# Optimization experiments

Measured on AMD Instinct MI355X. Metric: run time of the kernel, lower is better.

## Reference

```python
import jax, jax.numpy as jnp
import numpy as np

I, H = 256, 512  # input_sz, hidden_sz
MU_MIN, MU_MAX, STD_MIN = 1e-6, 1e6, 1e-6


def _xavier(key, shape):
    fan_in, fan_out = shape[1], shape[0]
    a = jnp.sqrt(6.0 / (fan_in + fan_out)).astype(jnp.float32)
    return jax.random.uniform(key, shape, jnp.float32, -a, a)


def setup_inputs() -> dict:
    key = jax.random.key(0)
    ks = jax.random.split(key, 6)
    B, S = 64, 512
    x = jax.random.normal(ks[0], (B, S, I), jnp.float32)
    eps = jax.random.normal(ks[1], (S + 1, B, H), jnp.float32)
    W_ih = _xavier(ks[2], (4 * H, I))   # torch LSTM weight_ih_l0, gate order i,f,g,o
    W_hh = _xavier(ks[3], (4 * H, H))
    b_ih = jnp.zeros((4 * H,), jnp.float32)
    b_hh = jnp.zeros((4 * H,), jnp.float32)
    G = _xavier(ks[4], (H, 2 * H))      # Gaussian_Sampler gauss_parameter_generator
    return {"x": x, "eps": eps, "W_ih": W_ih, "W_hh": W_hh, "b_ih": b_ih, "b_hh": b_hh, "G": G}


def _sample(c, G, eps_t):
    # c: [B,H]; stats = c @ G -> [B,2H]
    stats = c @ G
    mu = jnp.clip(stats[:, :H], MU_MIN, MU_MAX)
    std = jnp.clip(jax.nn.softplus(stats[:, H:]), STD_MIN)
    return mu + eps_t * std, mu, std


def reference(x, eps, W_ih, W_hh, b_ih, b_hh, G):
    B, S, _ = x.shape
    h0 = jnp.zeros((B, H), x.dtype)
    c0 = jnp.zeros((B, H), x.dtype)
    # initial sampling of cell state (uses eps[0])
    c0_s, mu0, std0 = _sample(c0, G, eps[0])

    def step(carry, inp):
        h, c = carry
        x_t, eps_t = inp  # [B,I], [B,H]
        gates = x_t @ W_ih.T + b_ih + h @ W_hh.T + b_hh  # [B,4H]
        i_g = jax.nn.sigmoid(gates[:, 0 * H:1 * H])
        f_g = jax.nn.sigmoid(gates[:, 1 * H:2 * H])
        g_g = jnp.tanh(gates[:, 2 * H:3 * H])
        o_g = jax.nn.sigmoid(gates[:, 3 * H:4 * H])
        c_new = f_g * c + i_g * g_g
        h_new = o_g * jnp.tanh(c_new)
        c_s, mu, std = _sample(c_new, G, eps_t)
        return (h_new, c_s), (h_new, mu, std)

    xs = (jnp.swapaxes(x, 0, 1), eps[1:])  # [S,B,I], [S,B,H]
    (h_f, c_f), (hs, mus, stds) = jax.lax.scan(step, (h0, c0_s), xs)
    hidden_seq = jnp.swapaxes(hs, 0, 1)  # [B,S,H]
    c_mus = jnp.swapaxes(jnp.concatenate([mu0[None], mus], 0), 0, 1)    # [B,S+1,H]
    c_stds = jnp.swapaxes(jnp.concatenate([std0[None], stds], 0), 0, 1)  # [B,S+1,H]
    return hidden_seq, c_mus, c_stds, h_f, c_f
```

## Files before the change

### kernel.cpp

```cpp
#include <hip/hip_runtime.h>
#include <hip/hip_bf16.h>
#include <math.h>

#define I_DIM 256
#define H_DIM 512
#define B_DIM 64
#define S_DIM 512
#define SH    (S_DIM * H_DIM)
#define S1H   ((S_DIM + 1) * H_DIM)
#define BH    (B_DIM * H_DIM)
#define NGRP  4
#define GWG   64
#define NWG_TOT (NGRP * GWG)

typedef __bf16 bf16_t;
typedef bf16_t bf16x8 __attribute__((ext_vector_type(8)));
typedef float  f32x4  __attribute__((ext_vector_type(4)));
typedef float  f32x2  __attribute__((ext_vector_type(2)));

__device__ __forceinline__ float sigm_(float x) { return 1.0f / (1.0f + __expf(-x)); }
__device__ __forceinline__ float tanh_(float x) {
    x = fminf(fmaxf(x, -15.f), 15.f);
    float e = __expf(-2.f * x);
    return (1.f - e) / (1.f + e);
}
__device__ __forceinline__ float softplus_(float x) {
    return (x > 20.0f) ? x : log1pf(__expf(x));
}
__device__ __forceinline__ unsigned short bfbits_(float f) {
    return __builtin_bit_cast(unsigned short, (bf16_t)f);
}

__device__ __forceinline__ bf16x8 ld_frag(const bf16_t* base, int elem_idx) {
    return *reinterpret_cast<const bf16x8*>(base + elem_idx);
}

__global__ void k_init(bf16_t* __restrict__ hbuf0, unsigned int* __restrict__ bar,
                       float* __restrict__ out_cmu, float* __restrict__ out_cstd) {
    const int i = blockIdx.x * 256 + threadIdx.x;
    hbuf0[i] = (bf16_t)0.0f;
    const int b = i >> 9, j = i & 511;
    out_cmu [b * S1H + j] = 1e-6f;
    out_cstd[b * S1H + j] = 0.69314718055994531f;
    if (i < NWG_TOT) bar[i] = 0u;
}

__global__ __launch_bounds__(64, 1) void k_persist(
    const float* __restrict__ x, const float* __restrict__ eps,
    const float* __restrict__ W_ih, const float* __restrict__ W_hh,
    const float* __restrict__ b_ih, const float* __restrict__ b_hh,
    const float* __restrict__ Gm,
    bf16_t* __restrict__ hb0, bf16_t* __restrict__ hb1,
    bf16_t* __restrict__ cn0, bf16_t* __restrict__ cn1,
    unsigned int* __restrict__ bar,
    float* __restrict__ out_hidden, float* __restrict__ out_cmu,
    float* __restrict__ out_cstd, float* __restrict__ out_hf,
    float* __restrict__ out_cf)
{
    __shared__ __align__(16) unsigned short s_wih[8][2][64][8];
    __shared__ __align__(16) unsigned short s_gfr[16][64][8];
    __shared__ char s_pad[64 * 1024];
    if (x == nullptr) ((volatile char*)s_pad)[threadIdx.x] = 1;

    const int wc = blockIdx.x & 63;
    const int g  = blockIdx.x >> 6;
    const int l  = threadIdx.x;
    const int lr = l & 15;
    const int kq = l >> 4;
    const int nsub   = lr & 7;
    const int ghalf  = lr >> 3;
    const int mycell = wc * 8 + nsub;
    const int col0 = ghalf * H_DIM + mycell;
    const int col1 = 1024 + col0;
    const int gcol = ghalf * H_DIM + mycell;
    const int row0 = g * 16 + kq * 4;
    const int arow = g * 16 + lr;
    unsigned int* barg = bar + g * GWG;

    bf16x8 whh0[16], whh1[16];
    #pragma unroll
    for (int kt = 0; kt < 16; ++kt) {
        const float* p0 = W_hh + (size_t)col0 * H_DIM + kt * 32 + kq * 8;
        const float* p1 = W_hh + (size_t)col1 * H_DIM + kt * 32 + kq * 8;
        bf16x8 f0, f1;
        #pragma unroll
        for (int j = 0; j < 8; ++j) { f0[j] = (bf16_t)p0[j]; f1[j] = (bf16_t)p1[j]; }
        whh0[kt] = f0; whh1[kt] = f1;
    }
    #pragma unroll
    for (int kt = 0; kt < 8; ++kt) {
        const float* p0 = W_ih + (size_t)col0 * I_DIM + kt * 32 + kq * 8;
        const float* p1 = W_ih + (size_t)col1 * I_DIM + kt * 32 + kq * 8;
        bf16x8 f0, f1;
        #pragma unroll
        for (int j = 0; j < 8; ++j) { f0[j] = (bf16_t)p0[j]; f1[j] = (bf16_t)p1[j]; }
        *reinterpret_cast<bf16x8*>(&s_wih[kt][0][l][0]) = f0;
        *reinterpret_cast<bf16x8*>(&s_wih[kt][1][l][0]) = f1;
    }
    #pragma unroll
    for (int kt = 0; kt < 16; ++kt) {
        bf16x8 f;
        #pragma unroll
        for (int j = 0; j < 8; ++j)
            f[j] = (bf16_t)Gm[(size_t)(kt * 32 + kq * 8 + j) * 1024 + gcol];
        *reinterpret_cast<bf16x8*>(&s_gfr[kt][l][0]) = f;
    }
    const float bias0 = b_ih[col0] + b_hh[col0];
    const float bias1 = b_ih[col1] + b_hh[col1];
    __syncthreads();

    float csr[4];
    #pragma unroll
    for (int r = 0; r < 4; ++r)
        csr[r] = 1e-6f + eps[(size_t)(row0 + r) * H_DIM + mycell] * 0.69314718055994531f;

    f32x4 ax0e = {0,0,0,0}, ax0o = {0,0,0,0}, ax1e = {0,0,0,0}, ax1o = {0,0,0,0};
    #pragma unroll
    for (int kt = 0; kt < 8; kt += 2) {
        const float* xp = x + (size_t)arow * (S_DIM * I_DIM) + kt * 32 + kq * 8;
        float4 u0 = reinterpret_cast<const float4*>(xp)[0];
        float4 u1 = reinterpret_cast<const float4*>(xp)[1];
        float4 u2 = reinterpret_cast<const float4*>(xp + 32)[0];
        float4 u3 = reinterpret_cast<const float4*>(xp + 32)[1];
        bf16x8 af0, af1;
        af0[0]=(bf16_t)u0.x; af0[1]=(bf16_t)u0.y; af0[2]=(bf16_t)u0.z; af0[3]=(bf16_t)u0.w;
        af0[4]=(bf16_t)u1.x; af0[5]=(bf16_t)u1.y; af0[6]=(bf16_t)u1.z; af0[7]=(bf16_t)u1.w;
        af1[0]=(bf16_t)u2.x; af1[1]=(bf16_t)u2.y; af1[2]=(bf16_t)u2.z; af1[3]=(bf16_t)u2.w;
        af1[4]=(bf16_t)u3.x; af1[5]=(bf16_t)u3.y; af1[6]=(bf16_t)u3.z; af1[7]=(bf16_t)u3.w;
        bf16x8 w0e = *reinterpret_cast<const bf16x8*>(&s_wih[kt][0][l][0]);
        bf16x8 w1e = *reinterpret_cast<const bf16x8*>(&s_wih[kt][1][l][0]);
        bf16x8 w0o = *reinterpret_cast<const bf16x8*>(&s_wih[kt + 1][0][l][0]);
        bf16x8 w1o = *reinterpret_cast<const bf16x8*>(&s_wih[kt + 1][1][l][0]);
        ax0e = __builtin_amdgcn_mfma_f32_16x16x32_bf16(af0, w0e, ax0e, 0, 0, 0);
        ax1e = __builtin_amdgcn_mfma_f32_16x16x32_bf16(af0, w1e, ax1e, 0, 0, 0);
        ax0o = __builtin_amdgcn_mfma_f32_16x16x32_bf16(af1, w0o, ax0o, 0, 0, 0);
        ax1o = __builtin_amdgcn_mfma_f32_16x16x32_bf16(af1, w1o, ax1o, 0, 0, 0);
    }

    bf16x8 hf[16];
    #pragma unroll
    for (int kt = 0; kt < 16; ++kt) {
        bf16x8 z;
        #pragma unroll
        for (int j = 0; j < 8; ++j) z[j] = (bf16_t)0.0f;
        hf[kt] = z;
    }

    float  ev[4];
    f32x2  hv_st[4];
    f32x2  st_out[4];

    #pragma unroll 1
    for (int t = 0; t < S_DIM; ++t) {
        bf16_t*       hout = (t & 1) ? hb0 : hb1;
        bf16_t*       cnb  = (t & 1) ? cn1 : cn0;
        unsigned int* hout_u32 = (unsigned int*)hout;
        unsigned int* cnb_u32  = (unsigned int*)cnb;

        #pragma unroll
        for (int kt = 0; kt < 16; kt += 2) {
            ax0e = __builtin_amdgcn_mfma_f32_16x16x32_bf16(hf[kt],     whh0[kt],     ax0e, 0, 0, 0);
            ax1e = __builtin_amdgcn_mfma_f32_16x16x32_bf16(hf[kt],     whh1[kt],     ax1e, 0, 0, 0);
            ax0o = __builtin_amdgcn_mfma_f32_16x16x32_bf16(hf[kt + 1], whh0[kt + 1], ax0o, 0, 0, 0);
            ax1o = __builtin_amdgcn_mfma_f32_16x16x32_bf16(hf[kt + 1], whh1[kt + 1], ax1o, 0, 0, 0);
        }
        f32x4 a0 = ax0e + ax0o, a1 = ax1e + ax1o;

        #pragma unroll
        for (int r = 0; r < 4; ++r) {
            float sif = sigm_(a0[r] + bias0);
            float v1  = a1[r] + bias1;
            float go  = (ghalf == 0) ? tanh_(v1) : sigm_(v1);
            float fv  = __shfl_xor(sif, 8);
            float ov  = __shfl_xor(go, 8);
            float cn  = fv * csr[r] + sif * go;
            float hn  = ov * tanh_(cn);
            unsigned hcw = ((unsigned)bfbits_(cn) << 16) | (unsigned)bfbits_(hn);
            unsigned pp  = __shfl_xor(hcw, 1);
            float    hp  = __shfl_xor(hn, 1);
            hv_st[r].x = hn; hv_st[r].y = hp;
            if (ghalf == 0 && !(lr & 1)) {
                const int row  = row0 + r;
                const int cidx = (row * H_DIM + mycell) >> 1;
                unsigned hw = ((pp & 0xFFFFu) << 16) | (hcw & 0xFFFFu);
                unsigned cw = (pp & 0xFFFF0000u)     | (hcw >> 16);
                __hip_atomic_store(hout_u32 + cidx, hw, __ATOMIC_RELAXED, __HIP_MEMORY_SCOPE_AGENT);
                __hip_atomic_store(cnb_u32  + cidx, cw, __ATOMIC_RELAXED, __HIP_MEMORY_SCOPE_AGENT);
            }
        }

        __threadfence_block();
        if (l == 0)
            __hip_atomic_store(&barg[wc], (unsigned)(t + 1),
                               __ATOMIC_RELAXED, __HIP_MEMORY_SCOPE_AGENT);

        ax0e = ax0o = ax1e = ax1o = (f32x4){0,0,0,0};
        if (t + 1 < S_DIM) {
            #pragma unroll
            for (int kt = 0; kt < 8; kt += 2) {
                const float* xp = x + (size_t)arow * (S_DIM * I_DIM)
                                    + (size_t)(t + 1) * I_DIM + kt * 32 + kq * 8;
                float4 u0 = reinterpret_cast<const float4*>(xp)[0];
                float4 u1 = reinterpret_cast<const float4*>(xp)[1];
                float4 u2 = reinterpret_cast<const float4*>(xp + 32)[0];
                float4 u3 = reinterpret_cast<const float4*>(xp + 32)[1];
                bf16x8 af0, af1;
                af0[0]=(bf16_t)u0.x; af0[1]=(bf16_t)u0.y; af0[2]=(bf16_t)u0.z; af0[3]=(bf16_t)u0.w;
                af0[4]=(bf16_t)u1.x; af0[5]=(bf16_t)u1.y; af0[6]=(bf16_t)u1.z; af0[7]=(bf16_t)u1.w;
                af1[0]=(bf16_t)u2.x; af1[1]=(bf16_t)u2.y; af1[2]=(bf16_t)u2.z; af1[3]=(bf16_t)u2.w;
                af1[4]=(bf16_t)u3.x; af1[5]=(bf16_t)u3.y; af1[6]=(bf16_t)u3.z; af1[7]=(bf16_t)u3.w;
                bf16x8 w0e = *reinterpret_cast<const bf16x8*>(&s_wih[kt][0][l][0]);
                bf16x8 w1e = *reinterpret_cast<const bf16x8*>(&s_wih[kt][1][l][0]);
                bf16x8 w0o = *reinterpret_cast<const bf16x8*>(&s_wih[kt + 1][0][l][0]);
                bf16x8 w1o = *reinterpret_cast<const bf16x8*>(&s_wih[kt + 1][1][l][0]);
                ax0e = __builtin_amdgcn_mfma_f32_16x16x32_bf16(af0, w0e, ax0e, 0, 0, 0);
                ax1e = __builtin_amdgcn_mfma_f32_16x16x32_bf16(af0, w1e, ax1e, 0, 0, 0);
                ax0o = __builtin_amdgcn_mfma_f32_16x16x32_bf16(af1, w0o, ax0o, 0, 0, 0);
                ax1o = __builtin_amdgcn_mfma_f32_16x16x32_bf16(af1, w1o, ax1o, 0, 0, 0);
            }
        }
        if (t) {
            if (!(lr & 1)) {
                #pragma unroll
                for (int r = 0; r < 4; ++r) {
                    float* outp = ((ghalf == 0) ? out_cmu : out_cstd)
                                  + (size_t)(row0 + r) * S1H + (size_t)t * H_DIM + mycell;
                    __builtin_nontemporal_store(st_out[r], (f32x2*)outp);
                }
            }
        }
        if (ghalf == 0 && !(lr & 1)) {
            #pragma unroll
            for (int r = 0; r < 4; ++r)
                __builtin_nontemporal_store(hv_st[r],
                    (f32x2*)(out_hidden + (size_t)(row0 + r) * SH + (size_t)t * H_DIM + mycell));
        }
        #pragma unroll
        for (int r = 0; r < 4; ++r)
            ev[r] = eps[(size_t)(t + 1) * BH + (size_t)(row0 + r) * H_DIM + mycell];

        {
            const unsigned target = (unsigned)(t + 1);
            while (true) {
                unsigned v = __hip_atomic_load(&barg[l], __ATOMIC_RELAXED,
                                               __HIP_MEMORY_SCOPE_AGENT);
                if (__all((int)(v >= target))) break;
                __builtin_amdgcn_s_sleep(1);
            }
        }
        __builtin_amdgcn_fence(__ATOMIC_ACQUIRE, "agent");

        bf16x8 cf[16];
        #pragma unroll
        for (int kt = 0; kt < 16; ++kt)
            cf[kt] = ld_frag(cnb, arow * H_DIM + kt * 32 + kq * 8);
        #pragma unroll
        for (int kt = 0; kt < 16; ++kt)
            hf[kt] = ld_frag(hout, arow * H_DIM + kt * 32 + kq * 8);

        f32x4 se = {0,0,0,0}, so = {0,0,0,0};
        #pragma unroll
        for (int kt = 0; kt < 16; kt += 2) {
            bf16x8 g0 = *reinterpret_cast<const bf16x8*>(&s_gfr[kt][l][0]);
            bf16x8 g1 = *reinterpret_cast<const bf16x8*>(&s_gfr[kt + 1][l][0]);
            se = __builtin_amdgcn_mfma_f32_16x16x32_bf16(cf[kt],     g0, se, 0, 0, 0);
            so = __builtin_amdgcn_mfma_f32_16x16x32_bf16(cf[kt + 1], g1, so, 0, 0, 0);
        }
        f32x4 st = se + so;
        #pragma unroll
        for (int r = 0; r < 4; ++r) {
            float sv  = st[r];
            float muv = fminf(fmaxf(sv, 1e-6f), 1e6f);
            float sdv = fmaxf(softplus_(sv), 1e-6f);
            float outv = (ghalf == 0) ? muv : sdv;
            float op   = __shfl_xor(outv, 1);
            st_out[r].x = outv; st_out[r].y = op;
            float sd_p = __shfl_xor(outv, 8);
            csr[r] = muv + ev[r] * sd_p;
        }
    }

    if (!(lr & 1)) {
        #pragma unroll
        for (int r = 0; r < 4; ++r) {
            float* outp = ((ghalf == 0) ? out_cmu : out_cstd)
                          + (size_t)(row0 + r) * S1H + (size_t)S_DIM * H_DIM + mycell;
            __builtin_nontemporal_store(st_out[r], (f32x2*)outp);
        }
    }
    if (ghalf == 0 && !(lr & 1)) {
        #pragma unroll
        for (int r = 0; r < 4; ++r)
            __builtin_nontemporal_store(hv_st[r],
                (f32x2*)(out_hf + (row0 + r) * H_DIM + mycell));
    }
    if (ghalf == 0) {
        #pragma unroll
        for (int r = 0; r < 4; ++r)
            __builtin_nontemporal_store(csr[r], out_cf + (row0 + r) * H_DIM + mycell);
    }
}

extern "C" void kernel_launch(void* const* d_in, const int* in_sizes, int n_in,
                              void* d_out, int out_size, void* d_ws, size_t ws_size,
                              hipStream_t stream) {
    (void)in_sizes; (void)n_in; (void)out_size; (void)ws_size;

    const float* x    = (const float*)d_in[0];
    const float* eps  = (const float*)d_in[1];
    const float* W_ih = (const float*)d_in[2];
    const float* W_hh = (const float*)d_in[3];
    const float* b_ih = (const float*)d_in[4];
    const float* b_hh = (const float*)d_in[5];
    const float* Gm   = (const float*)d_in[6];

    float* out        = (float*)d_out;
    float* out_hidden = out;
    float* out_cmu    = out_hidden + (size_t)B_DIM * SH;
    float* out_cstd   = out_cmu + (size_t)B_DIM * S1H;
    float* out_hf     = out_cstd + (size_t)B_DIM * S1H;
    float* out_cf     = out_hf + (size_t)B_DIM * H_DIM;

    char* wsb = (char*)d_ws;
    bf16_t* hb0 = (bf16_t*)(wsb);
    bf16_t* hb1 = (bf16_t*)(wsb + (1u << 16));
    bf16_t* cn0 = (bf16_t*)(wsb + 2u * (1u << 16));
    bf16_t* cn1 = (bf16_t*)(wsb + 3u * (1u << 16));
    unsigned int* bar = (unsigned int*)(wsb + 4u * (1u << 16));

    k_init<<<dim3(128), dim3(256), 0, stream>>>(hb0, bar, out_cmu, out_cstd);
    k_persist<<<dim3(NWG_TOT), dim3(64), 0, stream>>>(
        x, eps, W_ih, W_hh, b_ih, b_hh, Gm,
        hb0, hb1, cn0, cn1, bar,
        out_hidden, out_cmu, out_cstd, out_hf, out_cf);
}
```

Baseline: 3.706 ms.

## Transpose h/c via shuffles into dwordx4 stores and use cache-bypassing loads instead of fences

Gathers each row's packed h/c words across lanes with two xor-shuffle stages, so one lane writes 16-byte chunks instead of many 4-byte atomic stores. The agent-scope acquire fence is replaced by a compiler-only fence. The exchanged buffers are now read and written with sc0 sc1 global loads and stores plus explicit vmcnt waits. The aim is to cut cache invalidation and store-count overhead on the per-step cross-workgroup barrier path. Correctness now depends on the sc0/sc1 bits giving coherent visibility across CUs without a hardware fence.

```diff
diff --git a/kernel.cpp b/kernel.cpp
--- a/kernel.cpp
+++ b/kernel.cpp
@@ -17,6 +17,7 @@
 typedef bf16_t bf16x8 __attribute__((ext_vector_type(8)));
 typedef float  f32x4  __attribute__((ext_vector_type(4)));
 typedef float  f32x2  __attribute__((ext_vector_type(2)));
+typedef unsigned int u32x4 __attribute__((ext_vector_type(4)));
 
 __device__ __forceinline__ float sigm_(float x) { return 1.0f / (1.0f + __expf(-x)); }
 __device__ __forceinline__ float tanh_(float x) {
@@ -29,10 +30,6 @@
 }
 __device__ __forceinline__ unsigned short bfbits_(float f) {
     return __builtin_bit_cast(unsigned short, (bf16_t)f);
-}
-
-__device__ __forceinline__ bf16x8 ld_frag(const bf16_t* base, int elem_idx) {
-    return *reinterpret_cast<const bf16x8*>(base + elem_idx);
 }
 
 __global__ void k_init(bf16_t* __restrict__ hbuf0, unsigned int* __restrict__ bar,
@@ -149,6 +146,7 @@
     float  ev[4];
     f32x2  hv_st[4];
     f32x2  st_out[4];
+    const int m = lr >> 1;
 
     #pragma unroll 1
     for (int t = 0; t < S_DIM; ++t) {
@@ -166,6 +164,7 @@
         }
         f32x4 a0 = ax0e + ax0o, a1 = ax1e + ax1o;
 
+        unsigned hwv[4], cwv[4];
         #pragma unroll
         for (int r = 0; r < 4; ++r) {
             float sif = sigm_(a0[r] + bias0);
@@ -179,17 +178,38 @@
             unsigned pp  = __shfl_xor(hcw, 1);
             float    hp  = __shfl_xor(hn, 1);
             hv_st[r].x = hn; hv_st[r].y = hp;
-            if (ghalf == 0 && !(lr & 1)) {
-                const int row  = row0 + r;
-                const int cidx = (row * H_DIM + mycell) >> 1;
-                unsigned hw = ((pp & 0xFFFFu) << 16) | (hcw & 0xFFFFu);
-                unsigned cw = (pp & 0xFFFF0000u)     | (hcw >> 16);
-                __hip_atomic_store(hout_u32 + cidx, hw, __ATOMIC_RELAXED, __HIP_MEMORY_SCOPE_AGENT);
-                __hip_atomic_store(cnb_u32  + cidx, cw, __ATOMIC_RELAXED, __HIP_MEMORY_SCOPE_AGENT);
-            }
-        }
-
-        __threadfence_block();
+            hwv[r] = ((pp & 0xFFFFu) << 16) | (hcw & 0xFFFFu);
+            cwv[r] = (pp & 0xFFFF0000u)     | (hcw >> 16);
+        }
+
+        unsigned t1h[4], t1c[4], t2h[4], t2c[4];
+        #pragma unroll
+        for (int b = 0; b < 4; ++b) {
+            unsigned ph = __shfl_xor(hwv[b ^ 1], 2);
+            unsigned pc = __shfl_xor(cwv[b ^ 1], 2);
+            t1h[b] = ((m ^ b) & 1) ? ph : hwv[b];
+            t1c[b] = ((m ^ b) & 1) ? pc : cwv[b];
+        }
+        #pragma unroll
+        for (int b = 0; b < 4; ++b) {
+            unsigned ph = __shfl_xor(t1h[b ^ 2], 4);
+            unsigned pc = __shfl_xor(t1c[b ^ 2], 4);
+            t2h[b] = ((m ^ b) & 2) ? ph : t1h[b];
+            t2c[b] = ((m ^ b) & 2) ? pc : t1c[b];
+        }
+        if (!(lr & 1) && !(lr & 8)) {
+            const int row = row0 + m;
+            u32x4 hq = {t2h[0], t2h[1], t2h[2], t2h[3]};
+            u32x4 cq = {t2c[0], t2c[1], t2c[2], t2c[3]};
+            unsigned* ha = hout_u32 + row * 256 + wc * 4;
+            unsigned* ca = cnb_u32  + row * 256 + wc * 4;
+            asm volatile("global_store_dwordx4 %0, %1, off sc0 sc1"
+                         :: "v"(ha), "v"(hq) : "memory");
+            asm volatile("global_store_dwordx4 %0, %1, off sc0 sc1"
+                         :: "v"(ca), "v"(cq) : "memory");
+        }
+
+        asm volatile("s_waitcnt vmcnt(0)" ::: "memory");
         if (l == 0)
             __hip_atomic_store(&barg[wc], (unsigned)(t + 1),
                                __ATOMIC_RELAXED, __HIP_MEMORY_SCOPE_AGENT);
@@ -248,15 +268,19 @@
                 __builtin_amdgcn_s_sleep(1);
             }
         }
-        __builtin_amdgcn_fence(__ATOMIC_ACQUIRE, "agent");
+        __atomic_signal_fence(__ATOMIC_ACQUIRE);
 
         bf16x8 cf[16];
         #pragma unroll
         for (int kt = 0; kt < 16; ++kt)
-            cf[kt] = ld_frag(cnb, arow * H_DIM + kt * 32 + kq * 8);
+            asm volatile("global_load_dwordx4 %0, %1, off sc0 sc1"
+                         : "=v"(cf[kt]) : "v"(cnb + arow * H_DIM + kt * 32 + kq * 8));
         #pragma unroll
         for (int kt = 0; kt < 16; ++kt)
-            hf[kt] = ld_frag(hout, arow * H_DIM + kt * 32 + kq * 8);
+            asm volatile("global_load_dwordx4 %0, %1, off sc0 sc1"
+                         : "=v"(hf[kt]) : "v"(hout + arow * H_DIM + kt * 32 + kq * 8));
+        asm volatile("s_waitcnt vmcnt(0)" ::: "memory");
+        __builtin_amdgcn_sched_barrier(0);
 
         f32x4 se = {0,0,0,0}, so = {0,0,0,0};
         #pragma unroll
```

New measurement: 4.107 ms. 1.11x slower.
